# Kernel tuning notes

Hardware: AMD Instinct MI355X
Metric: run time of the kernel (lower is better)

Reference implementation:

```python
import jax, jax.numpy as jnp
import numpy as np
from jax import lax

C = 256          # n_channels
DC = 2           # data_channel
GROUPS = 32      # GroupNorm32
EPS = 1e-5


def setup_inputs() -> dict:
    key = jax.random.key(0)
    ks = jax.random.split(key, 10)
    B, H, W = 32, 32, 32
    x = jax.random.normal(ks[0], (B, C, H, W), dtype=jnp.float32)
    cond_matrix = jax.random.normal(ks[1], (B, DC, 128, 128), dtype=jnp.float32)
    s = 0.02
    return {
        "x": x,
        "cond_matrix": cond_matrix,
        "gn_w": jnp.ones((C,), jnp.float32),
        "gn_b": jnp.zeros((C,), jnp.float32),
        "fp1_w": jax.random.normal(ks[2], (2 * C, C), jnp.float32) * s,  # feature_projection_1
        "fp1_b": jnp.zeros((2 * C,), jnp.float32),
        "fp2_w": jax.random.normal(ks[3], (C, DC), jnp.float32) * s,     # feature_projection_2
        "fp2_b": jnp.zeros((C,), jnp.float32),
        "out_w": jax.random.normal(ks[4], (C, C), jnp.float32) * s,
        "out_b": jnp.zeros((C,), jnp.float32),
    }


def _group_norm(x, w, b):
    # x: [B, C, H, W]
    B, Cc, H, W = x.shape
    xg = x.reshape(B, GROUPS, Cc // GROUPS, H * W)
    mean = xg.mean(axis=(2, 3), keepdims=True)
    var = xg.var(axis=(2, 3), keepdims=True)
    xg = (xg - mean) * lax.rsqrt(var + EPS)
    xn = xg.reshape(B, Cc, H * W)
    return xn * w[None, :, None] + b[None, :, None]  # [B, C, HW]


def reference(x, cond_matrix, gn_w, gn_b, fp1_w, fp1_b, fp2_w, fp2_b, out_w, out_b):
    B, Cc, H, W = x.shape
    f = cond_matrix.shape[-1] // W  # total downsample factor (two MaxPool2d(2,2) == one pool f x f)
    # cond_projection_1: stacked max-pools then SiLU
    q_ori = lax.reduce_window(cond_matrix, -jnp.inf, lax.max,
                              (1, 1, f, f), (1, 1, f, f), 'VALID')
    q_ori = jax.nn.silu(q_ori)
    q_ori = q_ori.reshape(B, DC, -1).transpose(0, 2, 1)        # [B, S, DC]
    q = q_ori @ fp2_w.T + fp2_b                                # [B, S, C]

    h2 = _group_norm(x, gn_w, gn_b).transpose(0, 2, 1)         # [B, S, C]
    kv = h2 @ fp1_w.T + fp1_b                                  # [B, S, 2C]
    k, v = jnp.split(kv, 2, axis=-1)

    scale = Cc ** -0.25
    attn = jnp.einsum('bid,bjd->bij', q * scale, k * scale)    # [B, S, S]
    attn = jax.nn.softmax(attn, axis=2)
    out = jnp.einsum('bij,bjd->bid', attn, v)                  # [B, S, C]
    out = out @ out_w.T + out_b
    out = out.transpose(0, 2, 1).reshape(B, Cc, H, W)
    return (out + x) / jnp.sqrt(2.0).astype(x.dtype)
```

## Files before the change

kernel.cpp:

```cpp
#include <hip/hip_runtime.h>
#include <math.h>

#define NB 32
#define NC 256
#define NS 1024
#define NG 32
#define EPSV 1e-5f
#define RS2 0.70710678118654752f
#define SC2 0.0625f

typedef __attribute__((ext_vector_type(8))) short s16x8;
typedef __attribute__((ext_vector_type(4))) float f32x4;
typedef __attribute__((ext_vector_type(4))) unsigned u32x4;

__device__ __forceinline__ unsigned short f2bf(float f) {
    unsigned u = __float_as_uint(f);
    return (unsigned short)((u + 0x7fffu + ((u >> 16) & 1u)) >> 16);
}
__device__ __forceinline__ float bf2f(unsigned u16) {
    return __uint_as_float(u16 << 16);
}
__device__ __forceinline__ unsigned cvtpk(float lo, float hi) {
    unsigned r;
    asm("v_cvt_pk_bf16_f32 %0, %1, %2" : "=v"(r) : "v"(lo), "v"(hi));
    return r;
}

__global__ __launch_bounds__(256) void k_front(const float* __restrict__ cond, float* __restrict__ qp,
                                               const float* __restrict__ x, float* __restrict__ mean,
                                               float* __restrict__ rstd,
                                               const float* __restrict__ out_w,
                                               const float* __restrict__ fp1w,
                                               const float* __restrict__ fp1b,
                                               const float* __restrict__ fp2w,
                                               const float* __restrict__ fp2b,
                                               unsigned short* __restrict__ w2b,
                                               float* __restrict__ b2,
                                               float* __restrict__ w0, float* __restrict__ w1,
                                               float* __restrict__ wb, float* __restrict__ zs) {
    __shared__ float ls[4], lss[4];
    __shared__ float ow[256];
    int blk = blockIdx.x, t = threadIdx.x;
    if (blk < 256) {
        int idx = blk * 256 + t;
        int ow_ = idx & 31, oh = (idx >> 5) & 31;
        int bd = idx >> 10;
        const float* src = cond + (((size_t)bd * 128 + oh * 4) * 128 + ow_ * 4);
        float m = -1e30f;
#pragma unroll
        for (int r = 0; r < 4; ++r) {
            float4 v4 = *reinterpret_cast<const float4*>(src + (size_t)r * 128);
            m = fmaxf(m, fmaxf(fmaxf(v4.x, v4.y), fmaxf(v4.z, v4.w)));
        }
        qp[idx] = m / (1.f + __expf(-m));
        return;
    }
    if (blk < 1280) {
        int bg = blk - 256;
        const float4* p = reinterpret_cast<const float4*>(x + (size_t)bg * 8192);
        float s = 0.f, ss = 0.f;
#pragma unroll
        for (int r = 0; r < 8; ++r) {
            float4 v4 = p[r * 256 + t];
            s  += v4.x + v4.y + v4.z + v4.w;
            ss += v4.x * v4.x + v4.y * v4.y + v4.z * v4.z + v4.w * v4.w;
        }
        for (int o = 32; o > 0; o >>= 1) { s += __shfl_xor(s, o); ss += __shfl_xor(ss, o); }
        int w = t >> 6;
        if ((t & 63) == 0) { ls[w] = s; lss[w] = ss; }
        __syncthreads();
        if (t == 0) {
            s = ls[0] + ls[1] + ls[2] + ls[3];
            ss = lss[0] + lss[1] + lss[2] + lss[3];
            float mn = s * (1.f / 8192.f);
            float var = ss * (1.f / 8192.f) - mn * mn;
            mean[bg] = mn;
            rstd[bg] = rsqrtf(var + EPSV);
        }
        return;
    }
    if (blk < 1536) {
        const float* fp1v = fp1w + 256 * 256;
        const float* fp1b_v = fp1b + 256;
        int c = blk - 1280;
        ow[t] = out_w[(size_t)c * 256 + t];
        __syncthreads();
        float acc = 0.f;
        for (int m = 0; m < 256; ++m) acc = fmaf(ow[m], fp1v[(size_t)m * 256 + t], acc);
        w2b[((t >> 5) << 13) + (c << 5) + (t & 31)] = f2bf(acc);
        float pb = ow[t] * fp1b_v[t];
        for (int o = 32; o > 0; o >>= 1) pb += __shfl_xor(pb, o);
        if ((t & 63) == 0) ls[t >> 6] = pb;
        __syncthreads();
        if (t == 0) b2[c] = ls[0] + ls[1] + ls[2] + ls[3];
        return;
    }
    int c = t;
    float a0 = 0.f, a1 = 0.f, ab = 0.f;
    for (int kk = 0; kk < 256; ++kk) {
        float f = fp1w[(size_t)kk * 256 + c];
        a0 += f * fp2w[kk * 2];
        a1 += f * fp2w[kk * 2 + 1];
        ab += f * fp2b[kk];
    }
    w0[c] = a0; w1[c] = a1; wb[c] = ab;
    if (c == 0) {
        float z0 = 0.f, z1 = 0.f, zb = 0.f;
        for (int kk = 0; kk < 256; ++kk) {
            float fb = fp1b[kk];
            z0 += fb * fp2w[kk * 2];
            z1 += fb * fp2w[kk * 2 + 1];
            zb += fb * fp2b[kk];
        }
        zs[0] = z0; zs[1] = z1; zs[2] = zb; zs[3] = 0.f;
    }
}

__global__ __launch_bounds__(256) void k_psi2(const float* __restrict__ x,
                                              const float* __restrict__ mean,
                                              const float* __restrict__ rstd,
                                              const float* __restrict__ gw,
                                              const float* __restrict__ gb,
                                              const float* __restrict__ w0,
                                              const float* __restrict__ w1,
                                              const float* __restrict__ wb,
                                              const float* __restrict__ zsp,
                                              float* __restrict__ Hpart,
                                              float* __restrict__ g1part) {
    int blk = blockIdx.x;
    int b = blk >> 4, sb = blk & 15, s0 = sb << 6;
    int t = threadIdx.x, w = t >> 6, l = t & 63;
    int lo16 = l & 15, ksl = l >> 4;
    __shared__ float sw0[256], sw1[256], swb[256];
    __shared__ float red[3][4][64];
    __shared__ float cns[4];
    __shared__ unsigned short psiT[16][72];

    {
        unsigned* pz = (unsigned*)psiT;
        for (int i = t; i < 576; i += 256) pz[i] = 0u;
    }
    {
        int c = t;
        int bg = b * NG + (c >> 3);
        float al = rstd[bg] * gw[c];
        float be = gb[c] - mean[bg] * al;
        sw0[c] = w0[c] * al; sw1[c] = w1[c] * al; swb[c] = wb[c] * al;
        float p0 = w0[c] * be, p1 = w1[c] * be, pb = wb[c] * be;
        for (int o = 32; o > 0; o >>= 1) {
            p0 += __shfl_xor(p0, o); p1 += __shfl_xor(p1, o); pb += __shfl_xor(pb, o);
        }
        if (l == 0) { red[0][w][0] = p0; red[1][w][0] = p1; red[2][w][0] = pb; }
    }
    __syncthreads();
    if (t == 0) {
        cns[0] = red[0][0][0] + red[0][1][0] + red[0][2][0] + red[0][3][0] + zsp[0];
        cns[1] = red[1][0][0] + red[1][1][0] + red[1][2][0] + red[1][3][0] + zsp[1];
        cns[2] = red[2][0][0] + red[2][1][0] + red[2][2][0] + red[2][3][0] + zsp[2];
    }
    __syncthreads();
    {
        float a0 = 0.f, a1 = 0.f, ab = 0.f;
        const float* xb = x + (((size_t)b) << 18) + s0 + l;
        int cb = w << 6;
#pragma unroll 8
        for (int cc = 0; cc < 64; ++cc) {
            float xv = xb[(size_t)(cb + cc) << 10];
            a0 = fmaf(sw0[cb + cc], xv, a0);
            a1 = fmaf(sw1[cb + cc], xv, a1);
            ab = fmaf(swb[cb + cc], xv, ab);
        }
        red[0][w][l] = a0; red[1][w][l] = a1; red[2][w][l] = ab;
    }
    __syncthreads();
    if (w == 0) {
        float A0 = red[0][0][l] + red[0][1][l] + red[0][2][l] + red[0][3][l];
        float A1 = red[1][0][l] + red[1][1][l] + red[1][2][l] + red[1][3][l];
        float AB = red[2][0][l] + red[2][1][l] + red[2][2][l] + red[2][3][l];
        float k0 = SC2 * (A0 + cns[0]);
        float k1 = SC2 * (A1 + cns[1]);
        float kb = SC2 * (AB + cns[2]);
        float eb = __expf(kb);
        float p[10];
        p[0] = eb; p[1] = eb * k0; p[2] = eb * k1;
        p[3] = 0.5f * p[1] * k0; p[4] = p[1] * k1; p[5] = 0.5f * p[2] * k1;
        p[6] = p[3] * k0 * (1.f / 3.f); p[7] = p[3] * k1;
        p[8] = p[5] * k0; p[9] = p[5] * k1 * (1.f / 3.f);
#pragma unroll
        for (int pi = 0; pi < 10; ++pi) psiT[pi][l] = f2bf(p[pi]);
#pragma unroll
        for (int pi = 0; pi < 10; ++pi)
            for (int o = 32; o > 0; o >>= 1) p[pi] += __shfl_xor(p[pi], o);
        if (l == 0) {
            float* gp = g1part + (size_t)(b * 16 + sb) * 16;
#pragma unroll
            for (int pi = 0; pi < 10; ++pi) gp[pi] = p[pi];
#pragma unroll
            for (int pi = 10; pi < 16; ++pi) gp[pi] = 0.f;
        }
    }
    __syncthreads();
    f32x4 acc[4];
    const f32x4 zero4 = {0.f, 0.f, 0.f, 0.f};
#pragma unroll
    for (int nt = 0; nt < 4; ++nt) acc[nt] = zero4;
#pragma unroll
    for (int ks = 0; ks < 2; ++ks) {
        s16x8 af = *(const s16x8*)&psiT[lo16][(ks << 5) + (ksl << 3)];
#pragma unroll
        for (int nt = 0; nt < 4; ++nt) {
            int n = (w << 6) + (nt << 4) + lo16;
            const float* xr = x + (((size_t)(b * 256 + n)) << 10) + s0 + (ks << 5) + (ksl << 3);
            float4 xa = *(const float4*)xr;
            float4 xc = *(const float4*)(xr + 4);
            u32x4 bp;
            bp[0] = cvtpk(xa.x, xa.y); bp[1] = cvtpk(xa.z, xa.w);
            bp[2] = cvtpk(xc.x, xc.y); bp[3] = cvtpk(xc.z, xc.w);
            acc[nt] = __builtin_amdgcn_mfma_f32_16x16x32_bf16(af, *(s16x8*)&bp, acc[nt], 0, 0, 0);
        }
    }
    float* hp = Hpart + (size_t)(b * 16 + sb) * 4096;
#pragma unroll
    for (int nt = 0; nt < 4; ++nt) {
        int n = (w << 6) + (nt << 4) + lo16;
#pragma unroll
        for (int reg = 0; reg < 4; ++reg) {
            int p = (ksl << 2) + reg;
            hp[p * 256 + n] = acc[nt][reg];
        }
    }
}

__global__ __launch_bounds__(256) void k_G2(const float* __restrict__ Hpart,
                                            const float* __restrict__ g1part,
                                            const float* __restrict__ mean,
                                            const float* __restrict__ rstd,
                                            const float* __restrict__ gw,
                                            const float* __restrict__ gb,
                                            const unsigned short* __restrict__ w2b,
                                            const float* __restrict__ b2,
                                            float* __restrict__ Gg,
                                            float* __restrict__ g1g) {
    int b = blockIdx.x, t = threadIdx.x;
    int w = t >> 6, l = t & 63, lo16 = l & 15, ksl = l >> 4;
    __shared__ unsigned short HLb[16][264];
    __shared__ float g1s[16];

    if (t < 16) {
        float s = 0.f;
        const float* gp = g1part + (size_t)b * 256 + t;
#pragma unroll
        for (int sb = 0; sb < 16; ++sb) s += gp[sb * 16];
        g1s[t] = s;
    }
    __syncthreads();

    {
        const float* hp = Hpart + (size_t)b * 65536;
        int n = t;
        int bg = b * NG + (n >> 3);
        float al = rstd[bg] * gw[n];
        float be = gb[n] - mean[bg] * al;
#pragma unroll
        for (int p = 0; p < 16; ++p) {
            float s = 0.f;
#pragma unroll
            for (int sb = 0; sb < 16; ++sb) s += hp[sb * 4096 + p * 256 + n];
            HLb[p][n] = f2bf(fmaf(al, s, be * g1s[p]));
        }
    }
    __syncthreads();

    f32x4 acc2[4];
    const f32x4 zero4 = {0.f, 0.f, 0.f, 0.f};
#pragma unroll
    for (int nt = 0; nt < 4; ++nt) acc2[nt] = zero4;
    for (int ks2 = 0; ks2 < 8; ++ks2) {
        s16x8 af2 = *(const s16x8*)&HLb[lo16][(ks2 << 5) + (ksl << 3)];
#pragma unroll
        for (int nt = 0; nt < 4; ++nt) {
            int c = (w << 6) + (nt << 4) + lo16;
            s16x8 bf = *(const s16x8*)&w2b[(ks2 << 13) + (c << 5) + (ksl << 3)];
            acc2[nt] = __builtin_amdgcn_mfma_f32_16x16x32_bf16(af2, bf, acc2[nt], 0, 0, 0);
        }
    }
#pragma unroll
    for (int nt = 0; nt < 4; ++nt) {
        int c = (w << 6) + (nt << 4) + lo16;
        float b2v = b2[c];
#pragma unroll
        for (int reg = 0; reg < 4; ++reg) {
            int p = (ksl << 2) + reg;
            if (p < 10) Gg[(b << 12) + (c << 4) + p] = acc2[nt][reg] + g1s[p] * b2v;
        }
    }
    if (t < 16) g1g[(b << 4) + t] = g1s[t];
}

__global__ __launch_bounds__(256) void k_out(const float* __restrict__ x,
                                             const float* __restrict__ qp,
                                             const float* __restrict__ Gg,
                                             const float* __restrict__ g1g,
                                             const float* __restrict__ out_b,
                                             float* __restrict__ dout) {
    int blk = blockIdx.x;
    int b = blk >> 5, c0 = (blk & 31) << 3;
    int t = threadIdx.x;
    __shared__ float Gs[128];
    __shared__ float g1l[10];
    __shared__ float obs[8];
    if (t < 128) Gs[t] = Gg[(b << 12) + (c0 << 4) + t];
    if (t < 10) g1l[t] = g1g[(b << 4) + t];
    if (t < 8)  obs[t] = out_b[c0 + t];
    __syncthreads();

    const float* qpa = qp + (((size_t)(b * 2)) << 10) + (t << 2);
    float4 qa4 = *(const float4*)qpa;
    float4 qb4 = *(const float4*)(qpa + 1024);
    float ph[4][10];
    float rd[4];
#pragma unroll
    for (int e = 0; e < 4; ++e) {
        float qa = ((const float*)&qa4)[e], qb = ((const float*)&qb4)[e];
        float qa2 = qa * qa, qb2 = qb * qb, qab = qa * qb;
        ph[e][0] = 1.f; ph[e][1] = qa; ph[e][2] = qb;
        ph[e][3] = qa2; ph[e][4] = qab; ph[e][5] = qb2;
        ph[e][6] = qa2 * qa; ph[e][7] = qa2 * qb; ph[e][8] = qa * qb2; ph[e][9] = qb2 * qb;
        float d = g1l[0];
#pragma unroll
        for (int p = 1; p < 10; ++p) d = fmaf(ph[e][p], g1l[p], d);
        float r;
        asm("v_rcp_f32 %0, %1" : "=v"(r) : "v"(d));
        r = r * (2.f - d * r);
        rd[e] = r;
    }
#pragma unroll
    for (int c = 0; c < 8; ++c) {
        const float* G = &Gs[c << 4];
        float ob = obs[c];
        size_t base = (((size_t)(b * 256 + c0 + c)) << 10) + (t << 2);
        float4 xv = *(const float4*)(x + base);
        float4 o4;
#pragma unroll
        for (int e = 0; e < 4; ++e) {
            float num = G[0];
#pragma unroll
            for (int p = 1; p < 10; ++p) num = fmaf(ph[e][p], G[p], num);
            ((float*)&o4)[e] = (num * rd[e] + ob + ((const float*)&xv)[e]) * RS2;
        }
        *(float4*)(dout + base) = o4;
    }
}

extern "C" void kernel_launch(void* const* d_in, const int* in_sizes, int n_in,
                              void* d_out, int out_size, void* d_ws, size_t ws_size,
                              hipStream_t stream) {
    const float* x     = (const float*)d_in[0];
    const float* cond  = (const float*)d_in[1];
    const float* gn_w  = (const float*)d_in[2];
    const float* gn_b  = (const float*)d_in[3];
    const float* fp1_w = (const float*)d_in[4];
    const float* fp1_b = (const float*)d_in[5];
    const float* fp2_w = (const float*)d_in[6];
    const float* fp2_b = (const float*)d_in[7];
    const float* out_w = (const float*)d_in[8];
    const float* out_b = (const float*)d_in[9];

    float* ws   = (float*)d_ws;
    float* qp   = ws;
    float* mean = ws + 65536;
    float* rstd = ws + 66560;
    float* w0   = ws + 67584;
    float* w1   = ws + 67840;
    float* wb   = ws + 68096;
    float* zs   = ws + 68352;
    float* b2   = ws + 68608;
    float* g1g  = ws + 68864;
    float* Gg   = ws + 69376;
    unsigned short* w2b = (unsigned short*)(ws + 200448);
    float* Hpart  = ws + 233216;
    float* g1part = ws + 2330368;

    k_front<<<1537, 256, 0, stream>>>(cond, qp, x, mean, rstd, out_w, fp1_w, fp1_b,
                                      fp2_w, fp2_b, w2b, b2, w0, w1, wb, zs);
    k_psi2<<<512, 256, 0, stream>>>(x, mean, rstd, gn_w, gn_b, w0, w1, wb, zs, Hpart, g1part);
    k_G2<<<32, 256, 0, stream>>>(Hpart, g1part, mean, rstd, gn_w, gn_b, w2b, b2, Gg, g1g);
    k_out<<<1024, 256, 0, stream>>>(x, qp, Gg, g1g, out_b, (float*)d_out);
}
```

Before: 65.65 us.

## Fuse k_G2 into k_psi3 via last-block-done atomic counter per batch

Removes the separate k_G2 launch by having each k_psi3 block increment a per-batch atomic counter after writing its partial H. The last block to finish for a batch performs the cross-block reduction and the second MFMA projection. The counters are zeroed in k_front. This saves one kernel launch and its boundary gap, at the cost of threadfences, extra shared memory in every block, and a serialized tail reduction done by 32 blocks. It also adds unroll pragmas to two weight-folding loops in k_front.

```diff
diff --git a/kernel.cpp b/kernel.cpp
--- a/kernel.cpp
+++ b/kernel.cpp
@@ -37,7 +37,8 @@
                                                unsigned short* __restrict__ w2b,
                                                float* __restrict__ b2,
                                                float* __restrict__ w0, float* __restrict__ w1,
-                                               float* __restrict__ wb, float* __restrict__ zs) {
+                                               float* __restrict__ wb, float* __restrict__ zs,
+                                               unsigned* __restrict__ done) {
     __shared__ float ls[4], lss[4];
     __shared__ float ow[256];
     int blk = blockIdx.x, t = threadIdx.x;
@@ -86,6 +87,7 @@
         ow[t] = out_w[(size_t)c * 256 + t];
         __syncthreads();
         float acc = 0.f;
+#pragma unroll 4
         for (int m = 0; m < 256; ++m) acc = fmaf(ow[m], fp1v[(size_t)m * 256 + t], acc);
         w2b[((t >> 5) << 13) + (c << 5) + (t & 31)] = f2bf(acc);
         float pb = ow[t] * fp1b_v[t];
@@ -95,8 +97,10 @@
         if (t == 0) b2[c] = ls[0] + ls[1] + ls[2] + ls[3];
         return;
     }
+    if (t < 32) done[t] = 0u;
     int c = t;
     float a0 = 0.f, a1 = 0.f, ab = 0.f;
+#pragma unroll 4
     for (int kk = 0; kk < 256; ++kk) {
         float f = fp1w[(size_t)kk * 256 + c];
         a0 += f * fp2w[kk * 2];
@@ -116,7 +120,7 @@
     }
 }
 
-__global__ __launch_bounds__(256) void k_psi2(const float* __restrict__ x,
+__global__ __launch_bounds__(256) void k_psi3(const float* __restrict__ x,
                                               const float* __restrict__ mean,
                                               const float* __restrict__ rstd,
                                               const float* __restrict__ gw,
@@ -125,8 +129,13 @@
                                               const float* __restrict__ w1,
                                               const float* __restrict__ wb,
                                               const float* __restrict__ zsp,
+                                              const unsigned short* __restrict__ w2b,
+                                              const float* __restrict__ b2,
                                               float* __restrict__ Hpart,
-                                              float* __restrict__ g1part) {
+                                              float* __restrict__ g1part,
+                                              unsigned* __restrict__ done,
+                                              float* __restrict__ Gg,
+                                              float* __restrict__ g1g) {
     int blk = blockIdx.x;
     int b = blk >> 4, sb = blk & 15, s0 = sb << 6;
     int t = threadIdx.x, w = t >> 6, l = t & 63;
@@ -135,6 +144,9 @@
     __shared__ float red[3][4][64];
     __shared__ float cns[4];
     __shared__ unsigned short psiT[16][72];
+    __shared__ unsigned short HLb[16][264];
+    __shared__ float g1s[16];
+    __shared__ unsigned isLastS;
 
     {
         unsigned* pz = (unsigned*)psiT;
@@ -200,61 +212,52 @@
         }
     }
     __syncthreads();
-    f32x4 acc[4];
-    const f32x4 zero4 = {0.f, 0.f, 0.f, 0.f};
-#pragma unroll
-    for (int nt = 0; nt < 4; ++nt) acc[nt] = zero4;
-#pragma unroll
-    for (int ks = 0; ks < 2; ++ks) {
-        s16x8 af = *(const s16x8*)&psiT[lo16][(ks << 5) + (ksl << 3)];
+    {
+        f32x4 acc[4];
+        const f32x4 zero4 = {0.f, 0.f, 0.f, 0.f};
+#pragma unroll
+        for (int nt = 0; nt < 4; ++nt) acc[nt] = zero4;
+#pragma unroll
+        for (int ks = 0; ks < 2; ++ks) {
+            s16x8 af = *(const s16x8*)&psiT[lo16][(ks << 5) + (ksl << 3)];
+#pragma unroll
+            for (int nt = 0; nt < 4; ++nt) {
+                int n = (w << 6) + (nt << 4) + lo16;
+                const float* xr = x + (((size_t)(b * 256 + n)) << 10) + s0 + (ks << 5) + (ksl << 3);
+                float4 xa = *(const float4*)xr;
+                float4 xc = *(const float4*)(xr + 4);
+                u32x4 bp;
+                bp[0] = cvtpk(xa.x, xa.y); bp[1] = cvtpk(xa.z, xa.w);
+                bp[2] = cvtpk(xc.x, xc.y); bp[3] = cvtpk(xc.z, xc.w);
+                acc[nt] = __builtin_amdgcn_mfma_f32_16x16x32_bf16(af, *(s16x8*)&bp, acc[nt], 0, 0, 0);
+            }
+        }
+        float* hp = Hpart + (size_t)(b * 16 + sb) * 4096;
 #pragma unroll
         for (int nt = 0; nt < 4; ++nt) {
             int n = (w << 6) + (nt << 4) + lo16;
-            const float* xr = x + (((size_t)(b * 256 + n)) << 10) + s0 + (ks << 5) + (ksl << 3);
-            float4 xa = *(const float4*)xr;
-            float4 xc = *(const float4*)(xr + 4);
-            u32x4 bp;
-            bp[0] = cvtpk(xa.x, xa.y); bp[1] = cvtpk(xa.z, xa.w);
-            bp[2] = cvtpk(xc.x, xc.y); bp[3] = cvtpk(xc.z, xc.w);
-            acc[nt] = __builtin_amdgcn_mfma_f32_16x16x32_bf16(af, *(s16x8*)&bp, acc[nt], 0, 0, 0);
-        }
-    }
-    float* hp = Hpart + (size_t)(b * 16 + sb) * 4096;
-#pragma unroll
-    for (int nt = 0; nt < 4; ++nt) {
-        int n = (w << 6) + (nt << 4) + lo16;
-#pragma unroll
-        for (int reg = 0; reg < 4; ++reg) {
-            int p = (ksl << 2) + reg;
-            hp[p * 256 + n] = acc[nt][reg];
-        }
-    }
-}
-
-__global__ __launch_bounds__(256) void k_G2(const float* __restrict__ Hpart,
-                                            const float* __restrict__ g1part,
-                                            const float* __restrict__ mean,
-                                            const float* __restrict__ rstd,
-                                            const float* __restrict__ gw,
-                                            const float* __restrict__ gb,
-                                            const unsigned short* __restrict__ w2b,
-                                            const float* __restrict__ b2,
-                                            float* __restrict__ Gg,
-                                            float* __restrict__ g1g) {
-    int b = blockIdx.x, t = threadIdx.x;
-    int w = t >> 6, l = t & 63, lo16 = l & 15, ksl = l >> 4;
-    __shared__ unsigned short HLb[16][264];
-    __shared__ float g1s[16];
+#pragma unroll
+            for (int reg = 0; reg < 4; ++reg) {
+                int p = (ksl << 2) + reg;
+                hp[p * 256 + n] = acc[nt][reg];
+            }
+        }
+    }
+
+    __threadfence();
+    if (t == 0) isLastS = (atomicAdd(&done[b], 1u) == 15u) ? 1u : 0u;
+    __syncthreads();
+    if (!isLastS) return;
+    __threadfence();
 
     if (t < 16) {
         float s = 0.f;
         const float* gp = g1part + (size_t)b * 256 + t;
 #pragma unroll
-        for (int sb = 0; sb < 16; ++sb) s += gp[sb * 16];
+        for (int sb2 = 0; sb2 < 16; ++sb2) s += gp[sb2 * 16];
         g1s[t] = s;
     }
     __syncthreads();
-
     {
         const float* hp = Hpart + (size_t)b * 65536;
         int n = t;
@@ -265,36 +268,37 @@
         for (int p = 0; p < 16; ++p) {
             float s = 0.f;
 #pragma unroll
-            for (int sb = 0; sb < 16; ++sb) s += hp[sb * 4096 + p * 256 + n];
+            for (int sb2 = 0; sb2 < 16; ++sb2) s += hp[sb2 * 4096 + p * 256 + n];
             HLb[p][n] = f2bf(fmaf(al, s, be * g1s[p]));
         }
     }
     __syncthreads();
-
-    f32x4 acc2[4];
-    const f32x4 zero4 = {0.f, 0.f, 0.f, 0.f};
-#pragma unroll
-    for (int nt = 0; nt < 4; ++nt) acc2[nt] = zero4;
-    for (int ks2 = 0; ks2 < 8; ++ks2) {
-        s16x8 af2 = *(const s16x8*)&HLb[lo16][(ks2 << 5) + (ksl << 3)];
+    {
+        f32x4 acc2[4];
+        const f32x4 zero4 = {0.f, 0.f, 0.f, 0.f};
+#pragma unroll
+        for (int nt = 0; nt < 4; ++nt) acc2[nt] = zero4;
+        for (int ks2 = 0; ks2 < 8; ++ks2) {
+            s16x8 af2 = *(const s16x8*)&HLb[lo16][(ks2 << 5) + (ksl << 3)];
+#pragma unroll
+            for (int nt = 0; nt < 4; ++nt) {
+                int c = (w << 6) + (nt << 4) + lo16;
+                s16x8 bf = *(const s16x8*)&w2b[(ks2 << 13) + (c << 5) + (ksl << 3)];
+                acc2[nt] = __builtin_amdgcn_mfma_f32_16x16x32_bf16(af2, bf, acc2[nt], 0, 0, 0);
+            }
+        }
 #pragma unroll
         for (int nt = 0; nt < 4; ++nt) {
             int c = (w << 6) + (nt << 4) + lo16;
-            s16x8 bf = *(const s16x8*)&w2b[(ks2 << 13) + (c << 5) + (ksl << 3)];
-            acc2[nt] = __builtin_amdgcn_mfma_f32_16x16x32_bf16(af2, bf, acc2[nt], 0, 0, 0);
-        }
-    }
-#pragma unroll
-    for (int nt = 0; nt < 4; ++nt) {
-        int c = (w << 6) + (nt << 4) + lo16;
-        float b2v = b2[c];
-#pragma unroll
-        for (int reg = 0; reg < 4; ++reg) {
-            int p = (ksl << 2) + reg;
-            if (p < 10) Gg[(b << 12) + (c << 4) + p] = acc2[nt][reg] + g1s[p] * b2v;
-        }
-    }
-    if (t < 16) g1g[(b << 4) + t] = g1s[t];
+            float b2v = b2[c];
+#pragma unroll
+            for (int reg = 0; reg < 4; ++reg) {
+                int p = (ksl << 2) + reg;
+                if (p < 10) Gg[(b << 12) + (c << 4) + p] = acc2[nt][reg] + g1s[p] * b2v;
+            }
+        }
+        if (t < 16) g1g[(b << 4) + t] = g1s[t];
+    }
 }
 
 __global__ __launch_bounds__(256) void k_out(const float* __restrict__ x,
@@ -380,10 +384,11 @@
     unsigned short* w2b = (unsigned short*)(ws + 200448);
     float* Hpart  = ws + 233216;
     float* g1part = ws + 2330368;
+    unsigned* done = (unsigned*)(ws + 2338560);
 
     k_front<<<1537, 256, 0, stream>>>(cond, qp, x, mean, rstd, out_w, fp1_w, fp1_b,
-                                      fp2_w, fp2_b, w2b, b2, w0, w1, wb, zs);
-    k_psi2<<<512, 256, 0, stream>>>(x, mean, rstd, gn_w, gn_b, w0, w1, wb, zs, Hpart, g1part);
-    k_G2<<<32, 256, 0, stream>>>(Hpart, g1part, mean, rstd, gn_w, gn_b, w2b, b2, Gg, g1g);
+                                      fp2_w, fp2_b, w2b, b2, w0, w1, wb, zs, done);
+    k_psi3<<<512, 256, 0, stream>>>(x, mean, rstd, gn_w, gn_b, w0, w1, wb, zs,
+                                    w2b, b2, Hpart, g1part, done, Gg, g1g);
     k_out<<<1024, 256, 0, stream>>>(x, qp, Gg, g1g, out_b, (float*)d_out);
 }
```

Result: slower. 193.2 us (+194.3%).
